# Kernel tuning notes

Measured on AMD Instinct MI355X. Metric: run time of the kernel, lower is better.

## Reference

```python
import jax, jax.numpy as jnp
import numpy as np

B, S, HID = 2, 2048, 1024
NH, HD = 16, 64  # num heads, head dim
NEG = 1e10

def setup_inputs() -> dict:
    key = jax.random.key(0)
    ks = jax.random.split(key, 4)
    scale = 1.0 / np.sqrt(HID)
    return {
        "hidden_states": jax.random.normal(ks[0], (B, S, HID), jnp.float32),
        "attention_mask": jnp.zeros((B, 1, 1, S), jnp.float32),
        "Wq": jax.random.normal(ks[1], (HID, HID), jnp.float32) * scale,
        "bq": jnp.zeros((HID,), jnp.float32),
        "Wk": jax.random.normal(ks[2], (HID, HID), jnp.float32) * scale,
        "bk": jnp.zeros((HID,), jnp.float32),
        "Wv": jax.random.normal(ks[3], (HID, HID), jnp.float32) * scale,
        "bv": jnp.zeros((HID,), jnp.float32),
    }

def _split_heads(x):
    # [B,S,HID] -> [B,NH,S,HD]
    return x.reshape(B, S, NH, HD).transpose(0, 2, 1, 3)

def reference(hidden_states, attention_mask, Wq, bq, Wk, bk, Wv, bv):
    q = _split_heads(hidden_states @ Wq.T + bq)
    k = _split_heads(hidden_states @ Wk.T + bk)
    v = _split_heads(hidden_states @ Wv.T + bv)
    scores = jnp.einsum("bhqd,bhkd->bhqk", q, k) / np.sqrt(HD)
    causal = jnp.tril(jnp.ones((S, S), jnp.float32))  # [S,S]
    scores = scores * causal - NEG * (1.0 - causal)
    scores = scores + attention_mask
    probs = jax.nn.softmax(scores, axis=-1)  # [B,NH,S,S]
    ctx = jnp.einsum("bhqk,bhkd->bhqd", probs, v)
    ctx = ctx.transpose(0, 2, 1, 3).reshape(B, S, HID)
    return (ctx, probs)
```

## Files before the change

kernel.cpp:

```cpp
#include <hip/hip_runtime.h>

#define S_LEN 2048
#define HIDN  1024
#define NHEAD 16
#define HDIM  64
#define NBATCH 2

typedef __bf16 bf16x8 __attribute__((ext_vector_type(8)));
typedef float  f32x4  __attribute__((ext_vector_type(4)));
typedef unsigned int  u32x4 __attribute__((ext_vector_type(4)));
typedef unsigned short u16;
typedef unsigned short u16x4 __attribute__((ext_vector_type(4)));

#define LOG2E      1.4426950408889634f
#define QS_L2E     0.18033688011112042f
#define NEG8_L2E  -11.541560327111707f

#define PSTR 68

__device__ __forceinline__ u16 f2bf(float f) {
    union { float f; unsigned int u; } v; v.f = f;
    unsigned int u = v.u;
    unsigned int r = ((u >> 16) & 1u) + 0x7FFFu;
    return (u16)((u + r) >> 16);
}

__device__ __forceinline__ f32x4 mfma16(bf16x8 a, bf16x8 b, f32x4 c) {
    return __builtin_amdgcn_mfma_f32_16x16x32_bf16(a, b, c, 0, 0, 0);
}

__device__ __forceinline__ f32x4 zf4() { f32x4 z = {0.f, 0.f, 0.f, 0.f}; return z; }

__device__ __forceinline__ bf16x8 pack8_trunc(f32x4 a, f32x4 b) {
    union { f32x4 f; u32x4 u; } ua, ub;
    ua.f = a; ub.f = b;
    union { unsigned int d[4]; bf16x8 v; } r;
    r.d[0] = __builtin_amdgcn_perm(ua.u.y, ua.u.x, 0x07060302u);
    r.d[1] = __builtin_amdgcn_perm(ua.u.w, ua.u.z, 0x07060302u);
    r.d[2] = __builtin_amdgcn_perm(ub.u.y, ub.u.x, 0x07060302u);
    r.d[3] = __builtin_amdgcn_perm(ub.u.w, ub.u.z, 0x07060302u);
    return r.v;
}

__device__ __forceinline__ void gld16(void* lds, const void* g) {
    __builtin_amdgcn_global_load_lds(
        (const __attribute__((address_space(1))) void*)g,
        (__attribute__((address_space(3))) void*)lds, 16, 0, 0);
}

__global__ __launch_bounds__(256) void cvt_all(
    const float* __restrict__ hs, const float* __restrict__ Wq,
    const float* __restrict__ Wk, const float* __restrict__ Wv,
    u16* __restrict__ hsb, u16* __restrict__ Wqb,
    u16* __restrict__ Wkb, u16* __restrict__ Wvb)
{
    const int NBH = (NBATCH * S_LEN * HIDN) / 1024;
    const int NBW = (HIDN * HIDN) / 1024;
    int bid = blockIdx.x;
    const float* __restrict__ s; u16* __restrict__ d;
    if (bid < NBH)                { s = hs; d = hsb; }
    else if (bid < NBH + NBW)     { s = Wq; d = Wqb; bid -= NBH; }
    else if (bid < NBH + 2 * NBW) { s = Wk; d = Wkb; bid -= NBH + NBW; }
    else                          { s = Wv; d = Wvb; bid -= NBH + 2 * NBW; }
    const int i = (bid * 256 + (int)threadIdx.x) * 4;
    float4 v = *(const float4*)&s[i];
    u16x4 o = { f2bf(v.x), f2bf(v.y), f2bf(v.z), f2bf(v.w) };
    *(u16x4*)&d[i] = o;
}

__global__ __launch_bounds__(256) void qkv_gemm(
    const u16* __restrict__ hsb,
    const u16* __restrict__ Wqb, const u16* __restrict__ Wkb, const u16* __restrict__ Wvb,
    const float* __restrict__ bq, const float* __restrict__ bk, const float* __restrict__ bv,
    u16* __restrict__ Qf, u16* __restrict__ Kf, u16* __restrict__ Vt)
{
    __shared__ u16 Rs[128 * 64];
    __shared__ u16 Cs[128 * 64];

    const int z = blockIdx.z;
    const u16*   __restrict__ W    = (z == 0) ? Wqb : (z == 1) ? Wkb : Wvb;
    const float* __restrict__ bias = (z == 0) ? bq  : (z == 1) ? bk  : bv;

    const int mbase = blockIdx.x * 128;
    const int nbase = blockIdx.y * 128;
    const u16* __restrict__ Rm = (z == 2) ? hsb : W;
    const u16* __restrict__ Cm = (z == 2) ? W   : hsb;
    const int rbase = (z == 2) ? mbase : nbase;
    const int cbase = (z == 2) ? nbase : mbase;

    const int tid  = threadIdx.x;
    const int lane = tid & 63;
    const int wv   = tid >> 6;
    const int wrow = wv >> 1, wcol = wv & 1;
    const int lrow = lane & 15, quad = lane >> 4;
    const int l7   = lrow & 7;

    const u16* rp[4]; const u16* cp[4];
#pragma unroll
    for (int t = 0; t < 4; ++t) {
        const int c = tid + t * 256;
        const int r = c >> 3;
        const int o = ((c & 7) ^ (r & 7)) * 8;
        rp[t] = &Rm[(size_t)(rbase + r) * HIDN + o];
        cp[t] = &Cm[(size_t)(cbase + r) * HIDN + o];
    }

    f32x4 acc[4][4];
#pragma unroll
    for (int i = 0; i < 4; ++i)
#pragma unroll
        for (int j = 0; j < 4; ++j) acc[i][j] = zf4();

    for (int k0 = 0; k0 < HIDN; k0 += 64) {
#pragma unroll
        for (int t = 0; t < 4; ++t) {
            gld16(&Rs[(tid + t * 256) * 8], rp[t] + k0);
            gld16(&Cs[(tid + t * 256) * 8], cp[t] + k0);
        }
        __syncthreads();
#pragma unroll
        for (int kk = 0; kk < 2; ++kk) {
            const int sc = ((kk * 4 + quad) ^ l7) * 8;
            bf16x8 af[4], bfr[4];
#pragma unroll
            for (int i = 0; i < 4; ++i)
                af[i] = *(const bf16x8*)&Rs[(wrow * 64 + i * 16 + lrow) * 64 + sc];
#pragma unroll
            for (int j = 0; j < 4; ++j)
                bfr[j] = *(const bf16x8*)&Cs[(wcol * 64 + j * 16 + lrow) * 64 + sc];
#pragma unroll
            for (int i = 0; i < 4; ++i)
#pragma unroll
                for (int j = 0; j < 4; ++j)
                    acc[i][j] = mfma16(af[i], bfr[j], acc[i][j]);
        }
        __syncthreads();
    }

    if (z == 2) {
        const int bb = mbase >> 11;
        const int sb = mbase & 2047;
#pragma unroll
        for (int i = 0; i < 4; ++i) {
#pragma unroll
            for (int j = 0; j < 4; ++j) {
                const int n = nbase + wcol * 64 + j * 16 + lrow;
                const int hh = n >> 6, d = n & 63;
                const float bs = bias[n];
                const int sbase = sb + wrow * 64 + i * 16 + quad * 4;
                u16x4 pk = { f2bf(acc[i][j][0] + bs), f2bf(acc[i][j][1] + bs),
                             f2bf(acc[i][j][2] + bs), f2bf(acc[i][j][3] + bs) };
                *(u16x4*)&Vt[(((size_t)(bb * NHEAD + hh)) * HDIM + d) * S_LEN + sbase] = pk;
            }
        }
    } else {
        u16* __restrict__ O = (z == 0) ? Qf : Kf;
#pragma unroll
        for (int i = 0; i < 4; ++i) {
#pragma unroll
            for (int j = 0; j < 4; ++j) {
                const int n0 = nbase + wrow * 64 + i * 16 + quad * 4;
                const int m  = mbase + wcol * 64 + j * 16 + lrow;
                const float4 b4 = *(const float4*)&bias[n0];
                u16x4 pk = { f2bf(acc[i][j][0] + b4.x), f2bf(acc[i][j][1] + b4.y),
                             f2bf(acc[i][j][2] + b4.z), f2bf(acc[i][j][3] + b4.w) };
                *(u16x4*)&O[(size_t)m * HIDN + n0] = pk;
            }
        }
    }
}

__global__ __launch_bounds__(256) void attn_kernel(
    const u16* __restrict__ Qf,
    const u16* __restrict__ Kf,
    const u16* __restrict__ Vt,
    const float* __restrict__ amask,
    float* __restrict__ ctx,
    float* __restrict__ probs)
{
    const int qt = 127 - blockIdx.x;
    const int h  = blockIdx.y;
    const int b  = blockIdx.z;
    const int bh = b * NHEAD + h;
    const int tid  = threadIdx.x;
    const int lane = tid & 63;
    const int wv   = tid >> 6;
    const int lrow = lane & 15, quad = lane >> 4;
    const int row0 = qt * 16;
    const int dti  = qt >> 2;
    const int nkt  = dti + 1;

    __shared__ float pfl[4][16 * PSTR];
    __shared__ float l_sh[4][16];

    {
        const int tail  = nkt * 64;
        const int nt4   = (S_LEN - tail) >> 2;
        const int r  = tid >> 4;
        const int c0 = tid & 15;
        const f32x4 zf = {0.f, 0.f, 0.f, 0.f};
        float* pr = &probs[((size_t)bh * S_LEN + row0 + r) * S_LEN + tail];
        for (int c4 = c0; c4 < nt4; c4 += 16)
            __builtin_nontemporal_store(zf, (f32x4*)&pr[c4 * 4]);
    }

    const u16* qp = &Qf[((size_t)b * S_LEN + row0 + lrow) * HIDN + h * HDIM + quad * 8];
    const bf16x8 qa0 = *(const bf16x8*)qp;
    const bf16x8 qa1 = *(const bf16x8*)(qp + 32);

    const float* __restrict__ am = &amask[(size_t)b * S_LEN];
    const u16* __restrict__ kbase = &Kf[(size_t)b * S_LEN * HIDN + h * HDIM + quad * 8];

    float l_lane[4] = {0.f, 0.f, 0.f, 0.f};
    for (int kt = wv; kt < nkt; kt += 4) {
        f32x4 c[4];
#pragma unroll
        for (int cb = 0; cb < 4; ++cb) {
            const int col = kt * 64 + cb * 16 + lrow;
            const u16* kp = kbase + (size_t)col * HIDN;
            bf16x8 kb0 = *(const bf16x8*)kp;
            bf16x8 kb1 = *(const bf16x8*)(kp + 32);
            c[cb] = mfma16(qa0, kb0, zf4());
            c[cb] = mfma16(qa1, kb1, c[cb]);
        }
        if (kt == dti) {
#pragma unroll
            for (int cb = 0; cb < 4; ++cb) {
                const int col = kt * 64 + cb * 16 + lrow;
                const float m8 = fmaf(am[col], LOG2E, NEG8_L2E);
#pragma unroll
                for (int reg = 0; reg < 4; ++reg) {
                    const int row = row0 + quad * 4 + reg;
                    const float e = exp2f(fmaf(c[cb][reg], QS_L2E, m8));
                    l_lane[reg] += (col <= row) ? e : 0.f;
                }
            }
        } else {
#pragma unroll
            for (int cb = 0; cb < 4; ++cb) {
                const int col = kt * 64 + cb * 16 + lrow;
                const float m8 = fmaf(am[col], LOG2E, NEG8_L2E);
#pragma unroll
                for (int reg = 0; reg < 4; ++reg)
                    l_lane[reg] += exp2f(fmaf(c[cb][reg], QS_L2E, m8));
            }
        }
    }
#pragma unroll
    for (int reg = 0; reg < 4; ++reg) {
#pragma unroll
        for (int off = 1; off < 16; off <<= 1)
            l_lane[reg] += __shfl_xor(l_lane[reg], off, 16);
    }
    if (lrow == 0) {
#pragma unroll
        for (int reg = 0; reg < 4; ++reg)
            l_sh[wv][quad * 4 + reg] = l_lane[reg];
    }
    __syncthreads();
    float inv_l[4];
#pragma unroll
    for (int reg = 0; reg < 4; ++reg) {
        const int rr = quad * 4 + reg;
        inv_l[reg] = 1.f / (l_sh[0][rr] + l_sh[1][rr] + l_sh[2][rr] + l_sh[3][rr]);
    }

    f32x4 av[4];
#pragma unroll
    for (int db = 0; db < 4; ++db) av[db] = zf4();

    float* __restrict__ pw = pfl[wv];
    const u16* __restrict__ vbase = &Vt[(size_t)bh * HDIM * S_LEN + quad * 8];

    for (int kt = wv; kt < nkt; kt += 4) {
        f32x4 c[4];
#pragma unroll
        for (int cb = 0; cb < 4; ++cb) {
            const int col = kt * 64 + cb * 16 + lrow;
            const u16* kp = kbase + (size_t)col * HIDN;
            bf16x8 kb0 = *(const bf16x8*)kp;
            bf16x8 kb1 = *(const bf16x8*)(kp + 32);
            c[cb] = mfma16(qa0, kb0, zf4());
            c[cb] = mfma16(qa1, kb1, c[cb]);
        }
        if (kt == dti) {
#pragma unroll
            for (int cb = 0; cb < 4; ++cb) {
                const int col = kt * 64 + cb * 16 + lrow;
                const float m8 = fmaf(am[col], LOG2E, NEG8_L2E);
#pragma unroll
                for (int reg = 0; reg < 4; ++reg) {
                    const int row = row0 + quad * 4 + reg;
                    const float p = (col <= row)
                        ? exp2f(fmaf(c[cb][reg], QS_L2E, m8)) * inv_l[reg] : 0.f;
                    pw[(quad * 4 + reg) * PSTR + cb * 16 + lrow] = p;
                }
            }
        } else {
#pragma unroll
            for (int cb = 0; cb < 4; ++cb) {
                const int col = kt * 64 + cb * 16 + lrow;
                const float m8 = fmaf(am[col], LOG2E, NEG8_L2E);
#pragma unroll
                for (int reg = 0; reg < 4; ++reg) {
                    const float p = exp2f(fmaf(c[cb][reg], QS_L2E, m8)) * inv_l[reg];
                    pw[(quad * 4 + reg) * PSTR + cb * 16 + lrow] = p;
                }
            }
        }

#pragma unroll
        for (int it = 0; it < 4; ++it) {
            const int r = it * 4 + quad;
            f32x4 v = *(const f32x4*)&pw[r * PSTR + lrow * 4];
            __builtin_nontemporal_store(
                v, (f32x4*)&probs[((size_t)bh * S_LEN + row0 + r) * S_LEN + kt * 64 + lrow * 4]);
        }

        f32x4 p0 = *(const f32x4*)&pw[lrow * PSTR + quad * 8];
        f32x4 p1 = *(const f32x4*)&pw[lrow * PSTR + quad * 8 + 4];
        f32x4 p2 = *(const f32x4*)&pw[lrow * PSTR + 32 + quad * 8];
        f32x4 p3 = *(const f32x4*)&pw[lrow * PSTR + 32 + quad * 8 + 4];
        bf16x8 pa0 = pack8_trunc(p0, p1);
        bf16x8 pa1 = pack8_trunc(p2, p3);
#pragma unroll
        for (int db = 0; db < 4; ++db) {
            const u16* vp = vbase + (size_t)(db * 16 + lrow) * S_LEN + kt * 64;
            bf16x8 vb0 = *(const bf16x8*)vp;
            bf16x8 vb1 = *(const bf16x8*)(vp + 32);
            av[db] = mfma16(pa0, vb0, av[db]);
            av[db] = mfma16(pa1, vb1, av[db]);
        }
    }

#pragma unroll
    for (int db = 0; db < 4; ++db)
#pragma unroll
        for (int reg = 0; reg < 4; ++reg)
            pw[lane * 16 + ((db * 4 + reg + (lane >> 1)) & 15)] = av[db][reg];
    __syncthreads();
#pragma unroll
    for (int reg = 0; reg < 4; ++reg) {
        const int sl = lane * 16 + ((wv * 4 + reg + (lane >> 1)) & 15);
        const float s = pfl[0][sl] + pfl[1][sl] + pfl[2][sl] + pfl[3][sl];
        __builtin_nontemporal_store(
            s, &ctx[((size_t)b * S_LEN + row0 + quad * 4 + reg) * HIDN + h * HDIM + wv * 16 + lrow]);
    }
}

extern "C" void kernel_launch(void* const* d_in, const int* in_sizes, int n_in,
                              void* d_out, int out_size, void* d_ws, size_t ws_size,
                              hipStream_t stream)
{
    const float* hs    = (const float*)d_in[0];
    const float* amask = (const float*)d_in[1];
    const float* Wq    = (const float*)d_in[2];
    const float* bq    = (const float*)d_in[3];
    const float* Wk    = (const float*)d_in[4];
    const float* bk    = (const float*)d_in[5];
    const float* Wv    = (const float*)d_in[6];
    const float* bv    = (const float*)d_in[7];

    float* out   = (float*)d_out;
    float* ctx   = out;
    float* probs = out + (size_t)NBATCH * S_LEN * HIDN;

    const size_t NTOK = (size_t)NBATCH * S_LEN;
    u16* hsb = (u16*)d_ws;
    u16* Wqb = hsb + NTOK * HIDN;
    u16* Wkb = Wqb + (size_t)HIDN * HIDN;
    u16* Wvb = Wkb + (size_t)HIDN * HIDN;
    u16* Qf  = Wvb + (size_t)HIDN * HIDN;
    u16* Kf  = Qf + NTOK * HIDN;
    u16* Vt  = Kf + NTOK * HIDN;

    const int nblk_cvt = (int)(NTOK * HIDN / 1024) + 3 * (HIDN * HIDN / 1024);
    cvt_all<<<nblk_cvt, 256, 0, stream>>>(hs, Wq, Wk, Wv, hsb, Wqb, Wkb, Wvb);

    qkv_gemm<<<dim3(32, 8, 3), 256, 0, stream>>>(hsb, Wqb, Wkb, Wvb, bq, bk, bv, Qf, Kf, Vt);
    attn_kernel<<<dim3(128, 16, 2), 256, 0, stream>>>(Qf, Kf, Vt, amask, ctx, probs);
}
```

Baseline: 768.8 us.

## Fuse Q, K, V projections into one GEMM sharing hidden-state tiles

```diff
diff --git a/kernel.cpp b/kernel.cpp
--- a/kernel.cpp
+++ b/kernel.cpp
@@ -68,103 +68,128 @@
     *(u16x4*)&d[i] = o;
 }
 
-__global__ __launch_bounds__(256) void qkv_gemm(
+__global__ __launch_bounds__(256) void qkv_fused(
     const u16* __restrict__ hsb,
     const u16* __restrict__ Wqb, const u16* __restrict__ Wkb, const u16* __restrict__ Wvb,
     const float* __restrict__ bq, const float* __restrict__ bk, const float* __restrict__ bv,
     u16* __restrict__ Qf, u16* __restrict__ Kf, u16* __restrict__ Vt)
 {
-    __shared__ u16 Rs[128 * 64];
-    __shared__ u16 Cs[128 * 64];
-
-    const int z = blockIdx.z;
-    const u16*   __restrict__ W    = (z == 0) ? Wqb : (z == 1) ? Wkb : Wvb;
-    const float* __restrict__ bias = (z == 0) ? bq  : (z == 1) ? bk  : bv;
+    __shared__ u16 As[128 * 64];
+    __shared__ u16 Bs[3][64 * 64];
 
     const int mbase = blockIdx.x * 128;
-    const int nbase = blockIdx.y * 128;
-    const u16* __restrict__ Rm = (z == 2) ? hsb : W;
-    const u16* __restrict__ Cm = (z == 2) ? W   : hsb;
-    const int rbase = (z == 2) ? mbase : nbase;
-    const int cbase = (z == 2) ? nbase : mbase;
-
+    const int nbase = blockIdx.y * 64;
     const int tid  = threadIdx.x;
     const int lane = tid & 63;
     const int wv   = tid >> 6;
-    const int wrow = wv >> 1, wcol = wv & 1;
+    const int wm   = wv >> 1, wn = wv & 1;
     const int lrow = lane & 15, quad = lane >> 4;
     const int l7   = lrow & 7;
 
-    const u16* rp[4]; const u16* cp[4];
+    const u16* __restrict__ Wm[3] = { Wqb, Wkb, Wvb };
+
+    const u16* ap[4];
 #pragma unroll
     for (int t = 0; t < 4; ++t) {
         const int c = tid + t * 256;
         const int r = c >> 3;
         const int o = ((c & 7) ^ (r & 7)) * 8;
-        rp[t] = &Rm[(size_t)(rbase + r) * HIDN + o];
-        cp[t] = &Cm[(size_t)(cbase + r) * HIDN + o];
-    }
-
-    f32x4 acc[4][4];
+        ap[t] = &hsb[(size_t)(mbase + r) * HIDN + o];
+    }
+    const u16* bp[3][2];
+#pragma unroll
+    for (int z = 0; z < 3; ++z)
+#pragma unroll
+        for (int t = 0; t < 2; ++t) {
+            const int c = tid + t * 256;
+            const int r = c >> 3;
+            const int o = ((c & 7) ^ (r & 7)) * 8;
+            bp[z][t] = &Wm[z][(size_t)(nbase + r) * HIDN + o];
+        }
+
+    f32x4 accqk[2][2][4];
+    f32x4 accv[4][2];
+#pragma unroll
+    for (int z = 0; z < 2; ++z)
+#pragma unroll
+        for (int j = 0; j < 2; ++j)
+#pragma unroll
+            for (int i = 0; i < 4; ++i) accqk[z][j][i] = zf4();
 #pragma unroll
     for (int i = 0; i < 4; ++i)
 #pragma unroll
-        for (int j = 0; j < 4; ++j) acc[i][j] = zf4();
+        for (int j = 0; j < 2; ++j) accv[i][j] = zf4();
 
     for (int k0 = 0; k0 < HIDN; k0 += 64) {
 #pragma unroll
-        for (int t = 0; t < 4; ++t) {
-            gld16(&Rs[(tid + t * 256) * 8], rp[t] + k0);
-            gld16(&Cs[(tid + t * 256) * 8], cp[t] + k0);
-        }
+        for (int t = 0; t < 4; ++t)
+            gld16(&As[(tid + t * 256) * 8], ap[t] + k0);
+#pragma unroll
+        for (int z = 0; z < 3; ++z)
+#pragma unroll
+            for (int t = 0; t < 2; ++t)
+                gld16(&Bs[z][(tid + t * 256) * 8], bp[z][t] + k0);
         __syncthreads();
+
 #pragma unroll
         for (int kk = 0; kk < 2; ++kk) {
             const int sc = ((kk * 4 + quad) ^ l7) * 8;
-            bf16x8 af[4], bfr[4];
+            bf16x8 hf[4], wf[3][2];
 #pragma unroll
             for (int i = 0; i < 4; ++i)
-                af[i] = *(const bf16x8*)&Rs[(wrow * 64 + i * 16 + lrow) * 64 + sc];
-#pragma unroll
-            for (int j = 0; j < 4; ++j)
-                bfr[j] = *(const bf16x8*)&Cs[(wcol * 64 + j * 16 + lrow) * 64 + sc];
+                hf[i] = *(const bf16x8*)&As[(wm * 64 + i * 16 + lrow) * 64 + sc];
+#pragma unroll
+            for (int z = 0; z < 3; ++z)
+#pragma unroll
+                for (int j = 0; j < 2; ++j)
+                    wf[z][j] = *(const bf16x8*)&Bs[z][(wn * 32 + j * 16 + lrow) * 64 + sc];
+#pragma unroll
+            for (int z = 0; z < 2; ++z)
+#pragma unroll
+                for (int j = 0; j < 2; ++j)
+#pragma unroll
+                    for (int i = 0; i < 4; ++i)
+                        accqk[z][j][i] = mfma16(wf[z][j], hf[i], accqk[z][j][i]);
 #pragma unroll
             for (int i = 0; i < 4; ++i)
 #pragma unroll
-                for (int j = 0; j < 4; ++j)
-                    acc[i][j] = mfma16(af[i], bfr[j], acc[i][j]);
+                for (int j = 0; j < 2; ++j)
+                    accv[i][j] = mfma16(hf[i], wf[2][j], accv[i][j]);
         }
         __syncthreads();
     }
 
-    if (z == 2) {
+#pragma unroll
+    for (int z = 0; z < 2; ++z) {
+        u16* __restrict__ O = (z == 0) ? Qf : Kf;
+        const float* __restrict__ bias = (z == 0) ? bq : bk;
+#pragma unroll
+        for (int j = 0; j < 2; ++j) {
+#pragma unroll
+            for (int i = 0; i < 4; ++i) {
+                const int n0 = nbase + wn * 32 + j * 16 + quad * 4;
+                const int m  = mbase + wm * 64 + i * 16 + lrow;
+                const float4 b4 = *(const float4*)&bias[n0];
+                u16x4 pk = { f2bf(accqk[z][j][i][0] + b4.x), f2bf(accqk[z][j][i][1] + b4.y),
+                             f2bf(accqk[z][j][i][2] + b4.z), f2bf(accqk[z][j][i][3] + b4.w) };
+                *(u16x4*)&O[(size_t)m * HIDN + n0] = pk;
+            }
+        }
+    }
+    {
         const int bb = mbase >> 11;
         const int sb = mbase & 2047;
 #pragma unroll
         for (int i = 0; i < 4; ++i) {
 #pragma unroll
-            for (int j = 0; j < 4; ++j) {
-                const int n = nbase + wcol * 64 + j * 16 + lrow;
+            for (int j = 0; j < 2; ++j) {
+                const int n = nbase + wn * 32 + j * 16 + lrow;
                 const int hh = n >> 6, d = n & 63;
-                const float bs = bias[n];
-                const int sbase = sb + wrow * 64 + i * 16 + quad * 4;
-                u16x4 pk = { f2bf(acc[i][j][0] + bs), f2bf(acc[i][j][1] + bs),
-                             f2bf(acc[i][j][2] + bs), f2bf(acc[i][j][3] + bs) };
-                *(u16x4*)&Vt[(((size_t)(bb * NHEAD + hh)) * HDIM + d) * S_LEN + sbase] = pk;
-            }
-        }
-    } else {
-        u16* __restrict__ O = (z == 0) ? Qf : Kf;
-#pragma unroll
-        for (int i = 0; i < 4; ++i) {
-#pragma unroll
-            for (int j = 0; j < 4; ++j) {
-                const int n0 = nbase + wrow * 64 + i * 16 + quad * 4;
-                const int m  = mbase + wcol * 64 + j * 16 + lrow;
-                const float4 b4 = *(const float4*)&bias[n0];
-                u16x4 pk = { f2bf(acc[i][j][0] + b4.x), f2bf(acc[i][j][1] + b4.y),
-                             f2bf(acc[i][j][2] + b4.z), f2bf(acc[i][j][3] + b4.w) };
-                *(u16x4*)&O[(size_t)m * HIDN + n0] = pk;
+                const float bs = bv[n];
+                const int s0 = sb + wm * 64 + i * 16 + quad * 4;
+                u16x4 pk = { f2bf(accv[i][j][0] + bs), f2bf(accv[i][j][1] + bs),
+                             f2bf(accv[i][j][2] + bs), f2bf(accv[i][j][3] + bs) };
+                *(u16x4*)&Vt[(((size_t)(bb * NHEAD + hh)) * HDIM + d) * S_LEN + s0] = pk;
             }
         }
     }
@@ -377,6 +402,6 @@
     const int nblk_cvt = (int)(NTOK * HIDN / 1024) + 3 * (HIDN * HIDN / 1024);
     cvt_all<<<nblk_cvt, 256, 0, stream>>>(hs, Wq, Wk, Wv, hsb, Wqb, Wkb, Wvb);
 
-    qkv_gemm<<<dim3(32, 8, 3), 256, 0, stream>>>(hsb, Wqb, Wkb, Wvb, bq, bk, bv, Qf, Kf, Vt);
+    qkv_fused<<<dim3(32, 16), 256, 0, stream>>>(hsb, Wqb, Wkb, Wvb, bq, bk, bv, Qf, Kf, Vt);
     attn_kernel<<<dim3(128, 16, 2), 256, 0, stream>>>(Qf, Kf, Vt, amask, ctx, probs);
 }
```

Result: no change. 762.1 us (-0.9%).
